# Kernel optimization log

Measured on AMD Instinct MI355X. Metric: run time of the kernel, lower is better.

The kernel has to match this reference:

```python
import jax, jax.numpy as jnp
import numpy as np

D_MODEL = 512
NUM_HEADS = 8
D_K = D_MODEL // NUM_HEADS
LN_EPS = 1e-5


def setup_inputs() -> dict:
    key = jax.random.key(0)
    ks = jax.random.split(key, 11)
    d = D_MODEL
    s = 1.0 / np.sqrt(d)
    return {
        "x": jax.random.normal(ks[0], (4, 2048, d), dtype=jnp.float32),
        "Wq": jax.random.uniform(ks[1], (d, d), jnp.float32, -s, s),
        "bq": jax.random.uniform(ks[2], (d,), jnp.float32, -s, s),
        "Wk": jax.random.uniform(ks[3], (d, d), jnp.float32, -s, s),
        "bk": jax.random.uniform(ks[4], (d,), jnp.float32, -s, s),
        "Wv": jax.random.uniform(ks[5], (d, d), jnp.float32, -s, s),
        "bv": jax.random.uniform(ks[6], (d,), jnp.float32, -s, s),
        "Wo": jax.random.uniform(ks[7], (d, d), jnp.float32, -s, s),
        "bo": jax.random.uniform(ks[8], (d,), jnp.float32, -s, s),
        "gamma": jnp.ones((d,), jnp.float32),
        "beta": jnp.zeros((d,), jnp.float32),
    }


def reference(x, Wq, bq, Wk, bk, Wv, bv, Wo, bo, gamma, beta):
    # x: (B, S, D). Dropout is identity (eval mode).
    B, S, D = x.shape
    H, dk = NUM_HEADS, D_K
    # Linear layers use torch convention: y = x @ W.T + b
    q = (x @ Wq.T + bq).reshape(B, S, H, dk).transpose(0, 2, 1, 3)  # (B,H,S,dk)
    k = (x @ Wk.T + bk).reshape(B, S, H, dk).transpose(0, 2, 1, 3)
    v = (x @ Wv.T + bv).reshape(B, S, H, dk).transpose(0, 2, 1, 3)
    scores = jnp.einsum("bhqd,bhkd->bhqk", q, k) / jnp.sqrt(jnp.float32(dk))
    attn = jax.nn.softmax(scores, axis=-1)
    ctx = jnp.einsum("bhqk,bhkd->bhqd", attn, v)  # (B,H,S,dk)
    ctx = ctx.transpose(0, 2, 1, 3).reshape(B, S, D)
    out = ctx @ Wo.T + bo
    # residual + LayerNorm
    y = x + out
    mu = jnp.mean(y, axis=-1, keepdims=True)
    var = jnp.mean(jnp.square(y - mu), axis=-1, keepdims=True)
    return (y - mu) / jnp.sqrt(var + LN_EPS) * gamma + beta
```

## Files before the change

kernel.cpp:

```cpp
#include <hip/hip_runtime.h>
#include <math.h>

#define D 512
#define NH 8
#define DK 64
#define S 2048
#define BATCH 4
#define N_TOK (BATCH * S)

#define QSCALE 0.18033688f

typedef __bf16 bf16x8 __attribute__((ext_vector_type(8)));
typedef __bf16 bf16x4 __attribute__((ext_vector_type(4)));
typedef float f32x4 __attribute__((ext_vector_type(4)));
typedef unsigned int u32x4 __attribute__((ext_vector_type(4)));

#define AS1 __attribute__((address_space(1)))
#define AS3 __attribute__((address_space(3)))

#define OFF_XB   0
#define OFF_WB   8388608
#define OFF_Q    10485760
#define OFF_K    18874368
#define OFF_VT   27262976
#define OFF_CTX  35651584
#define OFF_Y    10485760
#define OFF_FLAG 44040192

static __device__ __forceinline__ bf16x8 ldg8(const __bf16* p) {
    return *(const bf16x8*)p;
}
static __device__ __forceinline__ f32x4 mfma16(bf16x8 a, bf16x8 b, f32x4 c) {
    return __builtin_amdgcn_mfma_f32_16x16x32_bf16(a, b, c, 0, 0, 0);
}
static __device__ __forceinline__ float ldf(const void* p, size_t i, int isf) {
    return isf ? ((const float*)p)[i] : (float)(((const __bf16*)p)[i]);
}
static __device__ __forceinline__ float fexp2(float x) {
#if __has_builtin(__builtin_amdgcn_exp2f)
    return __builtin_amdgcn_exp2f(x);
#else
    return exp2f(x);
#endif
}
static __device__ __forceinline__ unsigned pack_trunc(float e0, float e1) {
    return (__builtin_bit_cast(unsigned, e0) >> 16)
         | (__builtin_bit_cast(unsigned, e1) & 0xFFFF0000u);
}
static __device__ __forceinline__ void gload_lds16(const void* g, void* l) {
    __builtin_amdgcn_global_load_lds((const AS1 char*)g, (AS3 char*)l, 16, 0, 0);
}

__global__ __launch_bounds__(256)
void cvt_kernel(const void* __restrict__ x,  const void* __restrict__ Wq,
                const void* __restrict__ Wk, const void* __restrict__ Wv,
                const void* __restrict__ Wo, __bf16* __restrict__ xb,
                __bf16* __restrict__ Wb, int* __restrict__ flag)
{
    const bf16x8 probe = ldg8((const __bf16*)x + (threadIdx.x & 63) * 8);
    int bad = 0;
#pragma unroll
    for (int j = 0; j < 8; ++j) bad |= !(fabsf((float)probe[j]) <= 64.0f);
    const int isf = __any(bad) ? 1 : 0;
    if (blockIdx.x == 0 && threadIdx.x == 0) *flag = isf;

    const size_t i0 = ((size_t)blockIdx.x * 256 + threadIdx.x) * 8;
    const void* src;
    __bf16* dst;
    size_t off;
    if (i0 < 4194304) {
        src = x; off = i0; dst = xb + i0;
    } else {
        const size_t wrel = i0 - 4194304;
        const size_t w = wrel >> 18;
        src = (w == 0) ? Wq : (w == 1) ? Wk : (w == 2) ? Wv : Wo;
        off = wrel & 262143;
        dst = Wb + wrel;
    }
    bf16x8 r;
    if (isf) {
        const float* f = (const float*)src + off;
#pragma unroll
        for (int j = 0; j < 8; ++j) r[j] = (__bf16)f[j];
    } else {
        r = *(const bf16x8*)((const __bf16*)src + off);
    }
    *(bf16x8*)dst = r;
}

__global__ __launch_bounds__(256)
void qkv_kernel(const __bf16* __restrict__ xb, const __bf16* __restrict__ Wb,
                const void* __restrict__ bq, const void* __restrict__ bk,
                const void* __restrict__ bv, const int* __restrict__ flag,
                __bf16* __restrict__ Q, __bf16* __restrict__ K,
                __bf16* __restrict__ Vt)
{
    __shared__ __align__(16) char smem[32768];

    const int isf = *flag;
    const int tid = threadIdx.x;
    const int w = tid >> 6, l = tid & 63;
    const int lane16 = l & 15, quad = l >> 4;
    const int wm = w >> 1, wn = w & 1;
    const int m0 = blockIdx.x * 128;
    const int by = blockIdx.y;
    const int n0 = by * 128;

    const int cwl = w * 64 + l;
    const int g0 = (cwl & 3) ^ ((cwl >> 3) & 3);
    const __bf16* aS0 = xb + (size_t)(m0 + (cwl >> 2)) * D + g0 * 8;
    const __bf16* aS1 = aS0 + (size_t)64 * D;
    const __bf16* bS0 = Wb + (size_t)(n0 + (cwl >> 2)) * D + g0 * 8;
    const __bf16* bS1 = bS0 + (size_t)64 * D;

    const int sw = (quad ^ ((lane16 >> 1) & 3)) * 16;
    const int aoff = (wm * 64 + lane16) * 64 + sw;
    const int boff = 8192 + (wn * 64 + lane16) * 64 + sw;

    f32x4 acc[4][4];
#pragma unroll
    for (int i = 0; i < 4; ++i)
#pragma unroll
        for (int j = 0; j < 4; ++j) acc[i][j] = (f32x4){0,0,0,0};

    gload_lds16(aS0, smem + w * 1024);
    gload_lds16(aS1, smem + 4096 + w * 1024);
    gload_lds16(bS0, smem + 8192 + w * 1024);
    gload_lds16(bS1, smem + 12288 + w * 1024);

    for (int kt = 0; kt < D / 32; ++kt) {
        __syncthreads();

        const char* bufp = smem + (kt & 1) * 16384;
        if (kt + 1 < D / 32) {
            char* nb = smem + ((kt + 1) & 1) * 16384;
            gload_lds16(aS0 + (kt + 1) * 32, nb + w * 1024);
            gload_lds16(aS1 + (kt + 1) * 32, nb + 4096 + w * 1024);
            gload_lds16(bS0 + (kt + 1) * 32, nb + 8192 + w * 1024);
            gload_lds16(bS1 + (kt + 1) * 32, nb + 12288 + w * 1024);
        }

        bf16x8 af[4], bf[4];
#pragma unroll
        for (int i = 0; i < 4; ++i) af[i] = *(const bf16x8*)(bufp + aoff + i * 1024);
#pragma unroll
        for (int j = 0; j < 4; ++j) bf[j] = *(const bf16x8*)(bufp + boff + j * 1024);
#pragma unroll
        for (int i = 0; i < 4; ++i)
#pragma unroll
            for (int j = 0; j < 4; ++j)
                acc[i][j] = mfma16(af[i], bf[j], acc[i][j]);
    }

    const int which = by >> 2;
    const int h = (by * 2 + wn) & 7;
    const float qs = (which == 0) ? QSCALE : 1.0f;
    const void* bias = (which == 0) ? bq : (which == 1) ? bk : bv;
    float bvv[4];
#pragma unroll
    for (int j = 0; j < 4; ++j)
        bvv[j] = ldf(bias, ((by & 3) * 128 + wn * 64 + 16 * j + lane16) & 511, isf);

    const int bb = m0 >> 11;
    const int ssb = (m0 & (S - 1)) + wm * 64;

    if (which < 2) {
        __bf16* out = ((which == 0) ? Q : K) + ((size_t)(bb * NH + h) * S) * DK;
#pragma unroll
        for (int i = 0; i < 4; ++i)
#pragma unroll
            for (int r = 0; r < 4; ++r) {
                const int ss = ssb + i * 16 + quad * 4 + r;
#pragma unroll
                for (int j = 0; j < 4; ++j)
                    out[(size_t)ss * DK + 16 * j + lane16] =
                        (__bf16)((acc[i][j][r] + bvv[j]) * qs);
            }
    } else {
#pragma unroll
        for (int i = 0; i < 4; ++i)
#pragma unroll
            for (int j = 0; j < 4; ++j) {
                const int dkc = 16 * j + lane16;
                __bf16* vp = Vt + ((size_t)(bb * NH + h) * DK + dkc) * S
                                + ssb + (quad + 4 * (i >> 1)) * 8 + 4 * (i & 1);
                bf16x4 pkt;
#pragma unroll
                for (int r = 0; r < 4; ++r) pkt[r] = (__bf16)(acc[i][j][r] + bvv[j]);
                *(bf16x4*)vp = pkt;
            }
    }
}

__global__ __launch_bounds__(512, 4)
void attn_kernel(const __bf16* __restrict__ Q, const __bf16* __restrict__ K,
                 const __bf16* __restrict__ Vt, __bf16* __restrict__ ctx)
{
    __shared__ __align__(16) char smem[65536];

    const int tid = threadIdx.x;
    const int w = tid >> 6, l = tid & 63;
    const int lane16 = l & 15, quad = l >> 4;
    const int team = w >> 2, tq = w & 3;

    const int lin = blockIdx.x;
    const int xcd = lin & 7;
    const int t = lin >> 3;
    const int bh = xcd * 4 + (t >> 4);
    const int qt = t & 15;
    const int b = bh >> 3, h = bh & 7;
    const size_t bhS = (size_t)bh * S;

    const int cwl = w * 64 + l;
    const int row = cwl >> 3;
    const int g = (cwl & 7) ^ (row & 7);
    const char* kS = (const char*)(K + (bhS + row) * DK) + g * 16;
    const char* vS = (const char*)(Vt + ((size_t)bh * DK + row) * S) + g * 16;

    const int qbase = qt * 128 + tq * 32;
    bf16x8 qa[2][2];
#pragma unroll
    for (int u = 0; u < 2; ++u) {
        const __bf16* Qp = Q + (bhS + qbase + u * 16 + lane16) * DK + quad * 8;
        qa[u][0] = ldg8(Qp);
        qa[u][1] = ldg8(Qp + 32);
    }

    bf16x8 aones;
#pragma unroll
    for (int j = 0; j < 8; ++j) aones[j] = (__bf16)1.0f;

    const int x7 = lane16 & 7;

    f32x4 o[2][4], lacc[2];
#pragma unroll
    for (int u = 0; u < 2; ++u) {
        lacc[u] = (f32x4){0,0,0,0};
#pragma unroll
        for (int tt = 0; tt < 4; ++tt) o[u][tt] = (f32x4){0,0,0,0};
    }

    gload_lds16(kS, smem + w * 1024);
    gload_lds16(vS, smem + 8192 + w * 1024);
    gload_lds16(kS + 8192, smem + 32768 + w * 1024);
    gload_lds16(vS + 128, smem + 32768 + 8192 + w * 1024);

    for (int p = 0; p < S / 128; ++p) {
        __syncthreads();

        const char* kb = smem + (team * 2 + (p & 1)) * 16384;
        const char* vb = kb + 8192;

        if (p + 1 < S / 128) {
            const int ns = (p + 1) & 1;
            const size_t c1 = 2 * p + 2, c2 = 2 * p + 3;
            char* b1 = smem + ns * 16384;
            char* b2 = smem + (2 + ns) * 16384;
            gload_lds16(kS + c1 * 8192, b1 + w * 1024);
            gload_lds16(vS + c1 * 128,  b1 + 8192 + w * 1024);
            gload_lds16(kS + c2 * 8192, b2 + w * 1024);
            gload_lds16(vS + c2 * 128,  b2 + 8192 + w * 1024);
        }

        f32x4 st[2][4];
#pragma unroll
        for (int tt = 0; tt < 4; ++tt) {
            const int base = (tt * 16 + lane16) * 128;
            const bf16x8 kfA = *(const bf16x8*)(kb + base + ((quad ^ x7) * 16));
            const bf16x8 kfB = *(const bf16x8*)(kb + base
                                                + (((quad + 4) ^ x7) * 16));
#pragma unroll
            for (int u = 0; u < 2; ++u) {
                f32x4 z = {0,0,0,0};
                z = mfma16(kfA, qa[u][0], z);
                st[u][tt] = mfma16(kfB, qa[u][1], z);
            }
        }

        bf16x8 bp[2][2];
#pragma unroll
        for (int u = 0; u < 2; ++u) {
            u32x4 u0, u1;
            u0[0] = pack_trunc(fexp2(st[u][0][0]), fexp2(st[u][0][1]));
            u0[1] = pack_trunc(fexp2(st[u][0][2]), fexp2(st[u][0][3]));
            u0[2] = pack_trunc(fexp2(st[u][1][0]), fexp2(st[u][1][1]));
            u0[3] = pack_trunc(fexp2(st[u][1][2]), fexp2(st[u][1][3]));
            u1[0] = pack_trunc(fexp2(st[u][2][0]), fexp2(st[u][2][1]));
            u1[1] = pack_trunc(fexp2(st[u][2][2]), fexp2(st[u][2][3]));
            u1[2] = pack_trunc(fexp2(st[u][3][0]), fexp2(st[u][3][1]));
            u1[3] = pack_trunc(fexp2(st[u][3][2]), fexp2(st[u][3][3]));
            bp[u][0] = __builtin_bit_cast(bf16x8, u0);
            bp[u][1] = __builtin_bit_cast(bf16x8, u1);
        }

#pragma unroll
        for (int tt = 0; tt < 4; ++tt) {
            const int base = (tt * 16 + lane16) * 128;
            const bf16x8 vA = *(const bf16x8*)(vb + base + ((quad ^ x7) * 16));
            const bf16x8 vB = *(const bf16x8*)(vb + base
                                               + (((quad + 4) ^ x7) * 16));
#pragma unroll
            for (int u = 0; u < 2; ++u) {
                o[u][tt] = mfma16(vA, bp[u][0], o[u][tt]);
                o[u][tt] = mfma16(vB, bp[u][1], o[u][tt]);
            }
        }
#pragma unroll
        for (int u = 0; u < 2; ++u) {
            lacc[u] = mfma16(aones, bp[u][0], lacc[u]);
            lacc[u] = mfma16(aones, bp[u][1], lacc[u]);
        }
    }

    __syncthreads();
    if (team == 1) {
        char* obase = smem + tq * 8192;
#pragma unroll
        for (int u = 0; u < 2; ++u)
#pragma unroll
            for (int tt = 0; tt < 4; ++tt)
                *(f32x4*)(obase + (u * 4 + tt) * 1024 + l * 16) = o[u][tt];
        float* lb = (float*)(smem + 32768 + tq * 512 + l * 8);
        lb[0] = lacc[0][0];
        lb[1] = lacc[1][0];
    }
    __syncthreads();
    if (team == 0) {
        const char* obase = smem + tq * 8192;
        const float* lb = (const float*)(smem + 32768 + tq * 512 + l * 8);
#pragma unroll
        for (int u = 0; u < 2; ++u) {
            const float inv = 1.0f / (lacc[u][0] + lb[u]);
            __bf16* cp = ctx + ((size_t)(b * S + qbase + u * 16 + lane16)) * D
                         + h * DK;
#pragma unroll
            for (int tt = 0; tt < 4; ++tt) {
                const f32x4 po = *(const f32x4*)(obase + (u * 4 + tt) * 1024
                                                 + l * 16);
                bf16x4 pkt;
#pragma unroll
                for (int r = 0; r < 4; ++r)
                    pkt[r] = (__bf16)((o[u][tt][r] + po[r]) * inv);
                *(bf16x4*)(cp + tt * 16 + quad * 4) = pkt;
            }
        }
    }
}

__global__ __launch_bounds__(256)
void proj_kernel(const __bf16* __restrict__ ctx, const __bf16* __restrict__ Wb,
                 const void* __restrict__ bo, const __bf16* __restrict__ xb,
                 const int* __restrict__ flag, __bf16* __restrict__ y)
{
    __shared__ __align__(16) char smem[24576];

    const int isf = *flag;
    const int tid = threadIdx.x;
    const int w = tid >> 6, l = tid & 63;
    const int lane16 = l & 15, quad = l >> 4;
    const int wm = w >> 1, wn = w & 1;
    const int m0 = blockIdx.x * 64;
    const int n0 = blockIdx.y * 128;

    const __bf16* Wo = Wb + (size_t)3 * 262144;
    const int cwl = w * 64 + l;
    const int g0 = (cwl & 3) ^ ((cwl >> 3) & 3);
    const __bf16* aS = ctx + (size_t)(m0 + (cwl >> 2)) * D + g0 * 8;
    const __bf16* bS0 = Wo + (size_t)(n0 + (cwl >> 2)) * D + g0 * 8;
    const __bf16* bS1 = bS0 + (size_t)64 * D;

    const int sw = (quad ^ ((lane16 >> 1) & 3)) * 16;
    const int aoff = (wm * 32 + lane16) * 64 + sw;
    const int boff = 4096 + (wn * 64 + lane16) * 64 + sw;

    f32x4 acc[2][4];
#pragma unroll
    for (int i = 0; i < 2; ++i)
#pragma unroll
        for (int j = 0; j < 4; ++j) acc[i][j] = (f32x4){0,0,0,0};

    gload_lds16(aS, smem + w * 1024);
    gload_lds16(bS0, smem + 4096 + w * 1024);
    gload_lds16(bS1, smem + 8192 + w * 1024);

    for (int kt = 0; kt < D / 32; ++kt) {
        __syncthreads();

        const char* bufp = smem + (kt & 1) * 12288;
        if (kt + 1 < D / 32) {
            char* nb = smem + ((kt + 1) & 1) * 12288;
            gload_lds16(aS + (kt + 1) * 32, nb + w * 1024);
            gload_lds16(bS0 + (kt + 1) * 32, nb + 4096 + w * 1024);
            gload_lds16(bS1 + (kt + 1) * 32, nb + 8192 + w * 1024);
        }

        bf16x8 af[2], bf[4];
#pragma unroll
        for (int i = 0; i < 2; ++i) af[i] = *(const bf16x8*)(bufp + aoff + i * 1024);
#pragma unroll
        for (int j = 0; j < 4; ++j) bf[j] = *(const bf16x8*)(bufp + boff + j * 1024);
#pragma unroll
        for (int i = 0; i < 2; ++i)
#pragma unroll
            for (int j = 0; j < 4; ++j)
                acc[i][j] = mfma16(af[i], bf[j], acc[i][j]);
    }

    float bvv[4];
#pragma unroll
    for (int j = 0; j < 4; ++j)
        bvv[j] = ldf(bo, n0 + wn * 64 + 16 * j + lane16, isf);

#pragma unroll
    for (int i = 0; i < 2; ++i)
#pragma unroll
        for (int r = 0; r < 4; ++r) {
            const int tok = m0 + wm * 32 + i * 16 + quad * 4 + r;
#pragma unroll
            for (int j = 0; j < 4; ++j) {
                const size_t idx = (size_t)tok * D + n0 + wn * 64 + 16 * j + lane16;
                y[idx] = (__bf16)(acc[i][j][r] + bvv[j] + (float)xb[idx]);
            }
        }
}

__global__ __launch_bounds__(256)
void ln_kernel(const __bf16* __restrict__ y, const void* __restrict__ gamma,
               const void* __restrict__ beta, const int* __restrict__ flag,
               void* __restrict__ out)
{
    const int isf = *flag;
    const int l = threadIdx.x & 63;
    const int tok = blockIdx.x * 4 + (threadIdx.x >> 6);
    const bf16x8 vv = ldg8(y + (size_t)tok * D + l * 8);

    float v[8];
    float sum = 0.f, sq = 0.f;
#pragma unroll
    for (int j = 0; j < 8; ++j) {
        v[j] = (float)vv[j];
        sum += v[j];
        sq  += v[j] * v[j];
    }
#pragma unroll
    for (int msk = 1; msk < 64; msk <<= 1) {
        sum += __shfl_xor(sum, msk);
        sq  += __shfl_xor(sq,  msk);
    }
    const float mean = sum * (1.0f / D);
    const float var  = sq * (1.0f / D) - mean * mean;
    const float rstd = rsqrtf(var + 1e-5f);

    const size_t base = (size_t)tok * D + l * 8;
#pragma unroll
    for (int j = 0; j < 8; ++j) {
        const float g  = ldf(gamma, l * 8 + j, isf);
        const float be = ldf(beta,  l * 8 + j, isf);
        const float r  = ((v[j] - mean) * rstd) * g + be;
        if (isf) ((float*)out)[base + j] = r;
        else     ((__bf16*)out)[base + j] = (__bf16)r;
    }
}

extern "C" void kernel_launch(void* const* d_in, const int* in_sizes, int n_in,
                              void* d_out, int out_size, void* d_ws,
                              size_t ws_size, hipStream_t stream)
{
    const void* x     = d_in[0];
    const void* Wq    = d_in[1];
    const void* bq    = d_in[2];
    const void* Wk    = d_in[3];
    const void* bk    = d_in[4];
    const void* Wv    = d_in[5];
    const void* bv    = d_in[6];
    const void* Wo    = d_in[7];
    const void* bo    = d_in[8];
    const void* gamma = d_in[9];
    const void* beta  = d_in[10];

    char* ws = (char*)d_ws;
    __bf16* xb  = (__bf16*)(ws + OFF_XB);
    __bf16* Wb  = (__bf16*)(ws + OFF_WB);
    __bf16* Qb  = (__bf16*)(ws + OFF_Q);
    __bf16* Kb  = (__bf16*)(ws + OFF_K);
    __bf16* Vtb = (__bf16*)(ws + OFF_VT);
    __bf16* ctx = (__bf16*)(ws + OFF_CTX);
    __bf16* y   = (__bf16*)(ws + OFF_Y);
    int*    flag = (int*)(ws + OFF_FLAG);

    cvt_kernel<<<5242880 / (256 * 8), 256, 0, stream>>>(
        x, Wq, Wk, Wv, Wo, xb, Wb, flag);
    qkv_kernel<<<dim3(N_TOK / 128, 12), 256, 0, stream>>>(
        xb, Wb, bq, bk, bv, flag, Qb, Kb, Vtb);
    attn_kernel<<<dim3(512), 512, 0, stream>>>(Qb, Kb, Vtb, ctx);
    proj_kernel<<<dim3(N_TOK / 64, 4), 256, 0, stream>>>(
        ctx, Wb, bo, xb, flag, y);
    ln_kernel<<<dim3(N_TOK / 4), 256, 0, stream>>>(y, gamma, beta, flag, d_out);
}
```

Measured before the change: 174.8 us.

## Fuse output projection with LayerNorm and add MFMA priority hints in attention

The output projection and residual+LayerNorm become one kernel. Each 512-thread block computes 16 full rows of 512 columns and reduces the row statistics through shared memory, which removes the bf16 y round-trip and one launch. The cost is that every block streams the whole Wo matrix, with 16-row tiles giving low reuse and 66KB of LDS limiting occupancy. Separately, the attention kernel wraps its MFMA groups in s_setprio to favour the matrix-issuing waves.

```diff
diff --git a/kernel.cpp b/kernel.cpp
--- a/kernel.cpp
+++ b/kernel.cpp
@@ -24,7 +24,6 @@
 #define OFF_K    18874368
 #define OFF_VT   27262976
 #define OFF_CTX  35651584
-#define OFF_Y    10485760
 #define OFF_FLAG 44040192
 
 static __device__ __forceinline__ bf16x8 ldg8(const __bf16* p) {
@@ -269,12 +268,14 @@
             const bf16x8 kfA = *(const bf16x8*)(kb + base + ((quad ^ x7) * 16));
             const bf16x8 kfB = *(const bf16x8*)(kb + base
                                                 + (((quad + 4) ^ x7) * 16));
+            __builtin_amdgcn_s_setprio(1);
 #pragma unroll
             for (int u = 0; u < 2; ++u) {
                 f32x4 z = {0,0,0,0};
                 z = mfma16(kfA, qa[u][0], z);
                 st[u][tt] = mfma16(kfB, qa[u][1], z);
             }
+            __builtin_amdgcn_s_setprio(0);
         }
 
         bf16x8 bp[2][2];
@@ -299,17 +300,21 @@
             const bf16x8 vA = *(const bf16x8*)(vb + base + ((quad ^ x7) * 16));
             const bf16x8 vB = *(const bf16x8*)(vb + base
                                                + (((quad + 4) ^ x7) * 16));
+            __builtin_amdgcn_s_setprio(1);
 #pragma unroll
             for (int u = 0; u < 2; ++u) {
                 o[u][tt] = mfma16(vA, bp[u][0], o[u][tt]);
                 o[u][tt] = mfma16(vB, bp[u][1], o[u][tt]);
             }
-        }
+            __builtin_amdgcn_s_setprio(0);
+        }
+        __builtin_amdgcn_s_setprio(1);
 #pragma unroll
         for (int u = 0; u < 2; ++u) {
             lacc[u] = mfma16(aones, bp[u][0], lacc[u]);
             lacc[u] = mfma16(aones, bp[u][1], lacc[u]);
         }
+        __builtin_amdgcn_s_setprio(0);
     }
 
     __syncthreads();
@@ -347,118 +352,136 @@
     }
 }
 
-__global__ __launch_bounds__(256)
-void proj_kernel(const __bf16* __restrict__ ctx, const __bf16* __restrict__ Wb,
-                 const void* __restrict__ bo, const __bf16* __restrict__ xb,
-                 const int* __restrict__ flag, __bf16* __restrict__ y)
+__global__ __launch_bounds__(512)
+void proj_ln_kernel(const __bf16* __restrict__ ctx, const __bf16* __restrict__ Wb,
+                    const void* __restrict__ bo, const __bf16* __restrict__ xb,
+                    const void* __restrict__ gamma, const void* __restrict__ beta,
+                    const int* __restrict__ flag, void* __restrict__ out)
 {
-    __shared__ __align__(16) char smem[24576];
+    __shared__ __align__(16) char smem[67584];
 
     const int isf = *flag;
     const int tid = threadIdx.x;
     const int w = tid >> 6, l = tid & 63;
     const int lane16 = l & 15, quad = l >> 4;
-    const int wm = w >> 1, wn = w & 1;
-    const int m0 = blockIdx.x * 64;
-    const int n0 = blockIdx.y * 128;
+    const int m0 = blockIdx.x * 16;
 
     const __bf16* Wo = Wb + (size_t)3 * 262144;
-    const int cwl = w * 64 + l;
-    const int g0 = (cwl & 3) ^ ((cwl >> 3) & 3);
-    const __bf16* aS = ctx + (size_t)(m0 + (cwl >> 2)) * D + g0 * 8;
-    const __bf16* bS0 = Wo + (size_t)(n0 + (cwl >> 2)) * D + g0 * 8;
-    const __bf16* bS1 = bS0 + (size_t)64 * D;
+    const int cwl = tid;
+
+    const int gA = (cwl & 3) ^ ((cwl >> 3) & 3);
+    const __bf16* aS = ctx + (size_t)(m0 + ((cwl & 63) >> 2)) * D + gA * 8;
+
+    const __bf16* bS[4];
+#pragma unroll
+    for (int c = 0; c < 4; ++c) {
+        const int s = c * 512 + cwl;
+        const int gB = (s & 3) ^ ((s >> 3) & 3);
+        bS[c] = Wo + (size_t)(s >> 2) * D + gB * 8;
+    }
 
     const int sw = (quad ^ ((lane16 >> 1) & 3)) * 16;
-    const int aoff = (wm * 32 + lane16) * 64 + sw;
-    const int boff = 4096 + (wn * 64 + lane16) * 64 + sw;
-
-    f32x4 acc[2][4];
-#pragma unroll
-    for (int i = 0; i < 2; ++i)
-#pragma unroll
-        for (int j = 0; j < 4; ++j) acc[i][j] = (f32x4){0,0,0,0};
-
-    gload_lds16(aS, smem + w * 1024);
-    gload_lds16(bS0, smem + 4096 + w * 1024);
-    gload_lds16(bS1, smem + 8192 + w * 1024);
+    const int aoff = lane16 * 64 + sw;
+    const int boff = 1024 + (w * 64 + lane16) * 64 + sw;
+
+    f32x4 acc[4];
+#pragma unroll
+    for (int j = 0; j < 4; ++j) acc[j] = (f32x4){0,0,0,0};
+
+    if (w == 0) gload_lds16(aS, smem);
+#pragma unroll
+    for (int c = 0; c < 4; ++c)
+        gload_lds16(bS[c], smem + 1024 + c * 8192 + w * 1024);
 
     for (int kt = 0; kt < D / 32; ++kt) {
         __syncthreads();
 
-        const char* bufp = smem + (kt & 1) * 12288;
+        const char* bufp = smem + (kt & 1) * 33792;
         if (kt + 1 < D / 32) {
-            char* nb = smem + ((kt + 1) & 1) * 12288;
-            gload_lds16(aS + (kt + 1) * 32, nb + w * 1024);
-            gload_lds16(bS0 + (kt + 1) * 32, nb + 4096 + w * 1024);
-            gload_lds16(bS1 + (kt + 1) * 32, nb + 8192 + w * 1024);
-        }
-
-        bf16x8 af[2], bf[4];
-#pragma unroll
-        for (int i = 0; i < 2; ++i) af[i] = *(const bf16x8*)(bufp + aoff + i * 1024);
+            char* nb = smem + ((kt + 1) & 1) * 33792;
+            if (w == 0) gload_lds16(aS + (kt + 1) * 32, nb);
+#pragma unroll
+            for (int c = 0; c < 4; ++c)
+                gload_lds16(bS[c] + (kt + 1) * 32,
+                            nb + 1024 + c * 8192 + w * 1024);
+        }
+
+        const bf16x8 af = *(const bf16x8*)(bufp + aoff);
+        bf16x8 bf[4];
 #pragma unroll
         for (int j = 0; j < 4; ++j) bf[j] = *(const bf16x8*)(bufp + boff + j * 1024);
 #pragma unroll
-        for (int i = 0; i < 2; ++i)
-#pragma unroll
-            for (int j = 0; j < 4; ++j)
-                acc[i][j] = mfma16(af[i], bf[j], acc[i][j]);
-    }
-
-    float bvv[4];
-#pragma unroll
-    for (int j = 0; j < 4; ++j)
-        bvv[j] = ldf(bo, n0 + wn * 64 + 16 * j + lane16, isf);
-
-#pragma unroll
-    for (int i = 0; i < 2; ++i)
-#pragma unroll
-        for (int r = 0; r < 4; ++r) {
-            const int tok = m0 + wm * 32 + i * 16 + quad * 4 + r;
-#pragma unroll
-            for (int j = 0; j < 4; ++j) {
-                const size_t idx = (size_t)tok * D + n0 + wn * 64 + 16 * j + lane16;
-                y[idx] = (__bf16)(acc[i][j][r] + bvv[j] + (float)xb[idx]);
-            }
-        }
-}
-
-__global__ __launch_bounds__(256)
-void ln_kernel(const __bf16* __restrict__ y, const void* __restrict__ gamma,
-               const void* __restrict__ beta, const int* __restrict__ flag,
-               void* __restrict__ out)
-{
-    const int isf = *flag;
-    const int l = threadIdx.x & 63;
-    const int tok = blockIdx.x * 4 + (threadIdx.x >> 6);
-    const bf16x8 vv = ldg8(y + (size_t)tok * D + l * 8);
-
-    float v[8];
-    float sum = 0.f, sq = 0.f;
-#pragma unroll
-    for (int j = 0; j < 8; ++j) {
-        v[j] = (float)vv[j];
-        sum += v[j];
-        sq  += v[j] * v[j];
-    }
-#pragma unroll
-    for (int msk = 1; msk < 64; msk <<= 1) {
-        sum += __shfl_xor(sum, msk);
-        sq  += __shfl_xor(sq,  msk);
-    }
-    const float mean = sum * (1.0f / D);
-    const float var  = sq * (1.0f / D) - mean * mean;
-    const float rstd = rsqrtf(var + 1e-5f);
-
-    const size_t base = (size_t)tok * D + l * 8;
-#pragma unroll
-    for (int j = 0; j < 8; ++j) {
-        const float g  = ldf(gamma, l * 8 + j, isf);
-        const float be = ldf(beta,  l * 8 + j, isf);
-        const float r  = ((v[j] - mean) * rstd) * g + be;
-        if (isf) ((float*)out)[base + j] = r;
-        else     ((__bf16*)out)[base + j] = (__bf16)r;
+        for (int j = 0; j < 4; ++j)
+            acc[j] = mfma16(af, bf[j], acc[j]);
+    }
+
+    float bvv[4], gv[4], bev[4];
+#pragma unroll
+    for (int j = 0; j < 4; ++j) {
+        const int col = w * 64 + 16 * j + lane16;
+        bvv[j] = ldf(bo, col, isf);
+        gv[j]  = ldf(gamma, col, isf);
+        bev[j] = ldf(beta, col, isf);
+    }
+
+    float v[4][4];
+#pragma unroll
+    for (int r = 0; r < 4; ++r) {
+        const int tok = m0 + quad * 4 + r;
+#pragma unroll
+        for (int j = 0; j < 4; ++j) {
+            const int col = w * 64 + 16 * j + lane16;
+            v[r][j] = acc[j][r] + bvv[j] + (float)xb[(size_t)tok * D + col];
+        }
+    }
+
+#pragma unroll
+    for (int r = 0; r < 4; ++r) {
+        float s1 = v[r][0] + v[r][1] + v[r][2] + v[r][3];
+        float s2 = v[r][0]*v[r][0] + v[r][1]*v[r][1]
+                 + v[r][2]*v[r][2] + v[r][3]*v[r][3];
+#pragma unroll
+        for (int msk = 1; msk < 16; msk <<= 1) {
+            s1 += __shfl_xor(s1, msk);
+            s2 += __shfl_xor(s2, msk);
+        }
+        if (lane16 == 0) {
+            float* pp = (float*)(smem + ((w * 16 + quad * 4 + r) * 8));
+            pp[0] = s1;
+            pp[1] = s2;
+        }
+    }
+    __syncthreads();
+
+    if (tid < 16) {
+        float s1 = 0.f, s2 = 0.f;
+#pragma unroll
+        for (int ww = 0; ww < 8; ++ww) {
+            const float* pp = (const float*)(smem + ((ww * 16 + tid) * 8));
+            s1 += pp[0];
+            s2 += pp[1];
+        }
+        const float mean = s1 * (1.0f / D);
+        const float var  = s2 * (1.0f / D) - mean * mean;
+        float* st = (float*)(smem + 2048 + tid * 8);
+        st[0] = mean;
+        st[1] = rsqrtf(var + 1e-5f);
+    }
+    __syncthreads();
+
+#pragma unroll
+    for (int r = 0; r < 4; ++r) {
+        const int row = quad * 4 + r;
+        const float* st = (const float*)(smem + 2048 + row * 8);
+        const float mean = st[0], rstd = st[1];
+        const size_t tb = (size_t)(m0 + row) * D;
+#pragma unroll
+        for (int j = 0; j < 4; ++j) {
+            const int col = w * 64 + 16 * j + lane16;
+            const float res = (v[r][j] - mean) * rstd * gv[j] + bev[j];
+            if (isf) ((float*)out)[tb + col] = res;
+            else     ((__bf16*)out)[tb + col] = (__bf16)res;
+        }
     }
 }
 
@@ -485,7 +508,6 @@
     __bf16* Kb  = (__bf16*)(ws + OFF_K);
     __bf16* Vtb = (__bf16*)(ws + OFF_VT);
     __bf16* ctx = (__bf16*)(ws + OFF_CTX);
-    __bf16* y   = (__bf16*)(ws + OFF_Y);
     int*    flag = (int*)(ws + OFF_FLAG);
 
     cvt_kernel<<<5242880 / (256 * 8), 256, 0, stream>>>(
@@ -493,7 +515,6 @@
     qkv_kernel<<<dim3(N_TOK / 128, 12), 256, 0, stream>>>(
         xb, Wb, bq, bk, bv, flag, Qb, Kb, Vtb);
     attn_kernel<<<dim3(512), 512, 0, stream>>>(Qb, Kb, Vtb, ctx);
-    proj_kernel<<<dim3(N_TOK / 64, 4), 256, 0, stream>>>(
-        ctx, Wb, bo, xb, flag, y);
-    ln_kernel<<<dim3(N_TOK / 4), 256, 0, stream>>>(y, gamma, beta, flag, d_out);
-}
+    proj_ln_kernel<<<dim3(N_TOK / 16), 512, 0, stream>>>(
+        ctx, Wb, bo, xb, gamma, beta, flag, d_out);
+}
```

After: 168.2 us, median of 2. -3.8%, faster.
